# Performance work log

Measured on AMD Instinct MI355X. Metric: run time of the kernel, lower is better.

Reference implementation:

```python
import jax, jax.numpy as jnp
import numpy as np

N_NODES = 100000
N_EDGES = 3200000
N_FEAT = 128
DIM = 64
N_GRAPHS = 4096
EPS = 1e-5


def setup_inputs() -> dict:
    key = jax.random.key(0)
    ks = jax.random.split(key, 20)
    x = jax.random.normal(ks[0], (N_NODES, N_FEAT), dtype=jnp.float32)
    edge_index = jax.random.randint(ks[1], (2, N_EDGES), 0, N_NODES, dtype=jnp.int64)
    batch = jnp.sort(jax.random.randint(ks[2], (N_NODES,), 0, N_GRAPHS, dtype=jnp.int64))
    s = 0.1
    inp = {
        "x": x, "edge_index": edge_index, "batch": batch,
        "w1": jax.random.normal(ks[3], (N_FEAT, DIM), jnp.float32) * s,
        "b1": jnp.zeros((DIM,), jnp.float32),
        "bn1_g": 1.0 + s * jax.random.normal(ks[4], (DIM,), jnp.float32),
        "bn1_b": s * jax.random.normal(ks[5], (DIM,), jnp.float32),
        "conv_w": jax.random.normal(ks[6], (3, DIM, DIM), jnp.float32) * s,
        "conv_b": jnp.zeros((3, DIM), jnp.float32),
        "bnc_g": 1.0 + s * jax.random.normal(ks[7], (3, DIM), jnp.float32),
        "bnc_b": s * jax.random.normal(ks[8], (3, DIM), jnp.float32),
        "mlp_w": jax.random.normal(ks[9], (3, DIM, DIM), jnp.float32) * s,
        "mlp_b": jnp.zeros((3, DIM), jnp.float32),
        "bnm_g": 1.0 + s * jax.random.normal(ks[10], (3, DIM), jnp.float32),
        "bnm_b": s * jax.random.normal(ks[11], (3, DIM), jnp.float32),
        "out_w": jax.random.normal(ks[12], (DIM, 1), jnp.float32) * s,
        "out_b": jnp.zeros((1,), jnp.float32),
    }
    return inp


def _batchnorm(h, g, b):
    # training-mode BN: batch stats over the node/graph axis, biased variance
    m = jnp.mean(h, axis=0)
    v = jnp.var(h, axis=0)
    return (h - m) * jax.lax.rsqrt(v + EPS) * g + b


def _forward(x, edge_index, batch, w1, b1, bn1_g, bn1_b, conv_w, conv_b,
             bnc_g, bnc_b, mlp_w, mlp_b, bnm_g, bnm_b, out_w, out_b):
    src, dst = edge_index[0], edge_index[1]
    n = x.shape[0]
    # degree with self-loops (GCNConv default: add_self_loops=True, sym norm)
    deg = jax.ops.segment_sum(jnp.ones((src.shape[0],), x.dtype), dst, num_segments=n) + 1.0
    dis = jax.lax.rsqrt(deg)                  # D^{-1/2}
    enorm = (dis[src] * dis[dst])[:, None]    # per-edge norm [E,1]
    self_norm = (dis * dis)[:, None]          # self-loop norm = 1/deg [N,1]

    def gcn(h, W, b):
        h = h @ W                                                  # lin first (PyG)
        agg = jax.ops.segment_sum(h[src] * enorm, dst, num_segments=n)
        return agg + h * self_norm + b

    h = _batchnorm(jax.nn.relu(gcn(x, w1, b1)), bn1_g, bn1_b)
    for i in range(3):
        h = _batchnorm(gcn(h, conv_w[i], conv_b[i]), bnc_g[i], bnc_b[i])
    p = jax.ops.segment_sum(h, batch, num_segments=N_GRAPHS)       # global_add_pool
    for i in range(3):
        p = _batchnorm(jax.nn.relu(p @ mlp_w[i] + mlp_b[i]), bnm_g[i], bnm_b[i])
        # dropout: eval mode -> identity
    return p @ out_w + out_b


def reference(x, edge_index, batch, w1, b1, bn1_g, bn1_b, conv_w, conv_b,
              bnc_g, bnc_b, mlp_w, mlp_b, bnm_g, bnm_b, out_w, out_b):
    return _forward(x, edge_index, batch, w1, b1, bn1_g, bn1_b, conv_w, conv_b,
                    bnc_g, bnc_b, mlp_w, mlp_b, bnm_g, bnm_b, out_w, out_b)
```

## Files before the change

### kernel.cpp

```cpp
#include <hip/hip_runtime.h>
#include <hip/hip_bf16.h>

#define N_FEAT 128
#define DIM 64


__global__ void hist_kernel(const int* __restrict__ dst, int E, int* __restrict__ cnt) {
    int e = blockIdx.x * blockDim.x + threadIdx.x;
    if (e < E) atomicAdd(&cnt[dst[e]], 1);
}

__global__ void dis_kernel(const int* __restrict__ cnt, float* __restrict__ dis, int N) {
    int i = blockIdx.x * blockDim.x + threadIdx.x;
    if (i < N) dis[i] = rsqrtf((float)cnt[i] + 1.0f);
}

__global__ void scanA_kernel(const int* __restrict__ cnt, int N,
                             int* __restrict__ tmp, int* __restrict__ blk) {
    __shared__ int ts[256];
    int t = threadIdx.x;
    int base = blockIdx.x * 1024 + t * 4;
    int v[4];
    int s = 0;
#pragma unroll
    for (int j = 0; j < 4; j++) {
        int i = base + j;
        v[j] = (i < N) ? ((cnt[i] + 7) & ~7) : 0;
        s += v[j];
    }
    ts[t] = s;
    __syncthreads();
    for (int off = 1; off < 256; off <<= 1) {
        int x = (t >= off) ? ts[t - off] : 0;
        __syncthreads();
        ts[t] += x;
        __syncthreads();
    }
    int run = ts[t] - s;
#pragma unroll
    for (int j = 0; j < 4; j++) {
        run += v[j];
        int i = base + j;
        if (i < N) tmp[i] = run;
    }
    if (t == 255) blk[blockIdx.x] = ts[255];
}

__global__ void scanB_kernel(int* __restrict__ blk, int nb) {
    __shared__ int ts[128];
    int t = threadIdx.x;
    int v = (t < nb) ? blk[t] : 0;
    ts[t] = v;
    __syncthreads();
    for (int off = 1; off < 128; off <<= 1) {
        int x = (t >= off) ? ts[t - off] : 0;
        __syncthreads();
        ts[t] += x;
        __syncthreads();
    }
    if (t < nb) blk[t] = ts[t] - v;
}

__global__ void scanC_kernel(const int* __restrict__ tmp, const int* __restrict__ blk,
                             const int* __restrict__ cnt,
                             int N, int* __restrict__ rowp, int* __restrict__ cur) {
    int i = blockIdx.x * blockDim.x + threadIdx.x;
    if (i < N) {
        int b = i >> 10;
        int local = i & 1023;
        int excl = blk[b] + (local ? tmp[i - 1] : 0);
        rowp[i] = excl;
        cur[i] = excl;
        if (i == N - 1) rowp[N] = excl + ((cnt[i] + 7) & ~7);
    }
}

__global__ void fill_kernel(const int* __restrict__ src, const int* __restrict__ dst, int E,
                            const float* __restrict__ dis, int* __restrict__ cur,
                            int2* __restrict__ ecw) {
    int e = blockIdx.x * blockDim.x + threadIdx.x;
    if (e < E) {
        int s = src[e], d = dst[e];
        int pos = atomicAdd(&cur[d], 1);
        ecw[pos] = make_int2(s << 8, __float_as_int(dis[s] * dis[d]));
    }
}

__global__ void pad_kernel(const int* __restrict__ cur, const int* __restrict__ rowp,
                           int2* __restrict__ ecw, int N) {
    int i = blockIdx.x * blockDim.x + threadIdx.x;
    if (i < N) {
        int p = cur[i], e = rowp[i + 1];
        for (; p < e; p++) ecw[p] = make_int2(0, 0);
    }
}


template<int K, bool AFFINE, bool BIAS, bool RELU, bool STATS>
__global__ __launch_bounds__(256) void gemm_kernel(
    const float* __restrict__ A, const float* __restrict__ W,
    const float* __restrict__ scale, const float* __restrict__ shift,
    const float* __restrict__ bias, float* __restrict__ C,
    float* __restrict__ stats, int M)
{
    __shared__ float As[64][K + 4];
    __shared__ float Ws[K][64];
    __shared__ float bs[64], bq[64];
    int t = threadIdx.x;
    int row0 = blockIdx.x * 64;

    for (int q = t; q < K * 16; q += 256) {
        int k = q >> 4, c4 = (q & 15) << 2;
        float4 w = *reinterpret_cast<const float4*>(&W[k * 64 + c4]);
        *reinterpret_cast<float4*>(&Ws[k][c4]) = w;
    }
    for (int q = t; q < 64 * (K / 4); q += 256) {
        int r = q / (K / 4);
        int k4 = (q % (K / 4)) * 4;
        int row = row0 + r;
        float4 a;
        if (row < M) {
            a = *reinterpret_cast<const float4*>(&A[(size_t)row * K + k4]);
            if (AFFINE) {
                a.x = a.x * scale[k4]     + shift[k4];
                a.y = a.y * scale[k4 + 1] + shift[k4 + 1];
                a.z = a.z * scale[k4 + 2] + shift[k4 + 2];
                a.w = a.w * scale[k4 + 3] + shift[k4 + 3];
            }
        } else {
            a = make_float4(0.f, 0.f, 0.f, 0.f);
        }
        *reinterpret_cast<float4*>(&As[r][k4]) = a;
    }
    __syncthreads();

    int ty = t >> 4, tx = t & 15;
    int r0 = ty * 4, c0 = tx * 4;
    float acc[4][4] = {};
#pragma unroll 2
    for (int k = 0; k < K; k += 4) {
        float4 A0 = *reinterpret_cast<const float4*>(&As[r0 + 0][k]);
        float4 A1 = *reinterpret_cast<const float4*>(&As[r0 + 1][k]);
        float4 A2 = *reinterpret_cast<const float4*>(&As[r0 + 2][k]);
        float4 A3 = *reinterpret_cast<const float4*>(&As[r0 + 3][k]);
        float ar[4][4] = {{A0.x, A0.y, A0.z, A0.w}, {A1.x, A1.y, A1.z, A1.w},
                          {A2.x, A2.y, A2.z, A2.w}, {A3.x, A3.y, A3.z, A3.w}};
#pragma unroll
        for (int kk = 0; kk < 4; kk++) {
            float4 w = *reinterpret_cast<const float4*>(&Ws[k + kk][c0]);
#pragma unroll
            for (int i = 0; i < 4; i++) {
                acc[i][0] += ar[i][kk] * w.x;
                acc[i][1] += ar[i][kk] * w.y;
                acc[i][2] += ar[i][kk] * w.z;
                acc[i][3] += ar[i][kk] * w.w;
            }
        }
    }

    if (STATS) {
        if (t < 64) { bs[t] = 0.f; bq[t] = 0.f; }
        __syncthreads();
    }
    float ssum[4] = {0.f, 0.f, 0.f, 0.f}, ssq[4] = {0.f, 0.f, 0.f, 0.f};
#pragma unroll
    for (int i = 0; i < 4; i++) {
        int row = row0 + r0 + i;
        if (row < M) {
            float4 v;
            float* vp = &v.x;
#pragma unroll
            for (int j = 0; j < 4; j++) {
                float x = acc[i][j];
                if (BIAS) x += bias[c0 + j];
                if (RELU) x = fmaxf(x, 0.f);
                vp[j] = x;
                if (STATS) { ssum[j] += x; ssq[j] += x * x; }
            }
            *reinterpret_cast<float4*>(&C[(size_t)row * 64 + c0]) = v;
        }
    }
    if (STATS) {
#pragma unroll
        for (int j = 0; j < 4; j++) {
            atomicAdd(&bs[c0 + j], ssum[j]);
            atomicAdd(&bq[c0 + j], ssq[j]);
        }
        __syncthreads();
        if (t < 64) {
            atomicAdd(&stats[t], bs[t]);
            atomicAdd(&stats[64 + t], bq[t]);
        }
    }
}


template<bool RELU>
__global__ __launch_bounds__(256) void agg_kernel(
    const float* __restrict__ H, const int* __restrict__ rowp,
    const int2* __restrict__ ecw,
    const float* __restrict__ dis, const float* __restrict__ bias,
    float* __restrict__ Hout, float* __restrict__ stats, int N)
{
    __shared__ float bs[64], bq[64];
    int t = threadIdx.x;
    int lane = t & 63;
    unsigned lane4 = (unsigned)lane << 2;
    const char* Hb = (const char*)H;
    int base = (blockIdx.x * 4 + (t >> 6)) * 8;
    float b = bias[lane];
    float ssum = 0.f, ssq = 0.f;
    for (int u = 0; u < 8; u++) {
        int n = base + u;
        if (n >= N) break;
        int e0 = rowp[n], e1 = rowp[n + 1];
        float acc = 0.f;
        for (int e = e0; e < e1; e += 8) {
            int2 p[8];
#pragma unroll
            for (int j = 0; j < 8; j++) p[j] = ecw[e + j];
            float h[8];
#pragma unroll
            for (int j = 0; j < 8; j++)
                h[j] = *(const float*)(Hb + ((unsigned)p[j].x + lane4));
#pragma unroll
            for (int j = 0; j < 8; j++)
                acc += h[j] * __int_as_float(p[j].y);
        }
        float dn = dis[n];
        acc += H[(size_t)n * 64 + lane] * (dn * dn);
        acc += b;
        if (RELU) acc = fmaxf(acc, 0.f);
        Hout[(size_t)n * 64 + lane] = acc;
        ssum += acc;
        ssq += acc * acc;
    }
    if (t < 64) { bs[t] = 0.f; bq[t] = 0.f; }
    __syncthreads();
    atomicAdd(&bs[lane], ssum);
    atomicAdd(&bq[lane], ssq);
    __syncthreads();
    if (t < 64) {
        atomicAdd(&stats[t], bs[t]);
        atomicAdd(&stats[64 + t], bq[t]);
    }
}


__global__ void bnprep_kernel(const float* __restrict__ stats, const float* __restrict__ g,
                              const float* __restrict__ b, float* __restrict__ ss, float cntInv) {
    int c = threadIdx.x;
    float mean = stats[c] * cntInv;
    float var = stats[64 + c] * cntInv - mean * mean;
    float sc = g[c] * rsqrtf(var + 1e-5f);
    ss[c] = sc;
    ss[64 + c] = b[c] - mean * sc;
}


__global__ __launch_bounds__(256) void pool_kernel(
    const float* __restrict__ H, const int* __restrict__ batch,
    const float* __restrict__ ss, float* __restrict__ P, int N)
{
    int t = threadIdx.x;
    int lane = t & 63;
    int base = (blockIdx.x * 4 + (t >> 6)) * 8;
    float sc = ss[lane], sh = ss[64 + lane];
    float acc = 0.f;
    int gprev = -1;
    for (int u = 0; u < 8; u++) {
        int n = base + u;
        if (n >= N) break;
        int g = batch[n];
        if (g != gprev) {
            if (gprev >= 0) atomicAdd(&P[(size_t)gprev * 64 + lane], acc);
            acc = 0.f;
            gprev = g;
        }
        acc += H[(size_t)n * 64 + lane] * sc + sh;
    }
    if (gprev >= 0) atomicAdd(&P[(size_t)gprev * 64 + lane], acc);
}


__global__ __launch_bounds__(256) void final_kernel(
    const float* __restrict__ P, const float* __restrict__ ss,
    const float* __restrict__ outw, const float* __restrict__ outb,
    float* __restrict__ out, int G)
{
    int t = threadIdx.x;
    int lane = t & 63;
    int g = blockIdx.x * 4 + (t >> 6);
    if (g >= G) return;
    float v = (P[(size_t)g * 64 + lane] * ss[lane] + ss[64 + lane]) * outw[lane];
#pragma unroll
    for (int off = 32; off >= 1; off >>= 1) v += __shfl_xor(v, off, 64);
    if (lane == 0) out[g] = v + outb[0];
}


extern "C" void kernel_launch(void* const* d_in, const int* in_sizes, int n_in,
                              void* d_out, int out_size, void* d_ws, size_t ws_size,
                              hipStream_t stream)
{
    const float* x      = (const float*)d_in[0];
    const int*   ei     = (const int*)d_in[1];
    const int*   batch  = (const int*)d_in[2];
    const float* w1     = (const float*)d_in[3];
    const float* b1     = (const float*)d_in[4];
    const float* bn1_g  = (const float*)d_in[5];
    const float* bn1_b  = (const float*)d_in[6];
    const float* conv_w = (const float*)d_in[7];
    const float* conv_b = (const float*)d_in[8];
    const float* bnc_g  = (const float*)d_in[9];
    const float* bnc_b  = (const float*)d_in[10];
    const float* mlp_w  = (const float*)d_in[11];
    const float* mlp_b  = (const float*)d_in[12];
    const float* bnm_g  = (const float*)d_in[13];
    const float* bnm_b  = (const float*)d_in[14];
    const float* out_w  = (const float*)d_in[15];
    const float* out_b  = (const float*)d_in[16];
    float* out = (float*)d_out;

    const int N = in_sizes[0] / N_FEAT;
    const int E = in_sizes[1] / 2;
    const int G = out_size;
    const int* esrc = ei;
    const int* edst = ei + E;

    char* ws = (char*)d_ws;
    size_t off = 0;
    auto alloc = [&](size_t bytes) {
        size_t cur = off;
        off += (bytes + 255) & ~(size_t)255;
        return (void*)(ws + cur);
    };

    int*   deg   = (int*)alloc((size_t)N * 4);
    float* dis   = (float*)alloc((size_t)N * 4);
    int*   rtmp  = (int*)alloc((size_t)N * 4);
    int*   rowp  = (int*)alloc((size_t)(N + 1) * 4);
    int*   cur   = (int*)alloc((size_t)N * 4);
    int*   blk   = (int*)alloc(256 * 4);
    int2*  ecw   = (int2*)alloc(((size_t)E + 8ull * N) * 8);
    float* bufA  = (float*)alloc((size_t)(N + 64) * 64 * 4);
    float* bufB  = (float*)alloc((size_t)(N + 64) * 64 * 4);
    float* stats = (float*)alloc(7 * 128 * 4);
    float* ssbuf = (float*)alloc(7 * 128 * 4);
    float* P     = (float*)alloc((size_t)G * 64 * 4);
    float* pA    = (float*)alloc((size_t)G * 64 * 4);
    float* pB    = (float*)alloc((size_t)G * 64 * 4);

    hipMemsetAsync(deg, 0, (size_t)N * 4, stream);
    hipMemsetAsync(stats, 0, 7 * 128 * 4, stream);
    hipMemsetAsync(P, 0, (size_t)G * 64 * 4, stream);

    hist_kernel<<<(E + 255) / 256, 256, 0, stream>>>(edst, E, deg);
    dis_kernel<<<(N + 255) / 256, 256, 0, stream>>>(deg, dis, N);
    int nchunk = (N + 1023) / 1024;
    scanA_kernel<<<nchunk, 256, 0, stream>>>(deg, N, rtmp, blk);
    scanB_kernel<<<1, 128, 0, stream>>>(blk, nchunk);
    scanC_kernel<<<(N + 255) / 256, 256, 0, stream>>>(rtmp, blk, deg, N, rowp, cur);
    fill_kernel<<<(E + 255) / 256, 256, 0, stream>>>(esrc, edst, E, dis, cur, ecw);
    pad_kernel<<<(N + 255) / 256, 256, 0, stream>>>(cur, rowp, ecw, N);

    int gemmN_grid = (N + 63) / 64;
    int aggN_grid = (N + 31) / 32;

    gemm_kernel<128, false, false, false, false><<<gemmN_grid, 256, 0, stream>>>(
        x, w1, nullptr, nullptr, nullptr, bufA, nullptr, N);
    agg_kernel<true><<<aggN_grid, 256, 0, stream>>>(
        bufA, rowp, ecw, dis, b1, bufB, stats, N);
    bnprep_kernel<<<1, 64, 0, stream>>>(stats, bn1_g, bn1_b, ssbuf, 1.0f / N);

    for (int i = 0; i < 3; i++) {
        const float* W  = conv_w + (size_t)i * 64 * 64;
        const float* bb = conv_b + (size_t)i * 64;
        float* st     = stats + (size_t)(1 + i) * 128;
        float* ss_in  = ssbuf + (size_t)i * 128;
        float* ss_out = ssbuf + (size_t)(1 + i) * 128;
        gemm_kernel<64, true, false, false, false><<<gemmN_grid, 256, 0, stream>>>(
            bufB, W, ss_in, ss_in + 64, nullptr, bufA, nullptr, N);
        agg_kernel<false><<<aggN_grid, 256, 0, stream>>>(
            bufA, rowp, ecw, dis, bb, bufB, st, N);
        bnprep_kernel<<<1, 64, 0, stream>>>(st, bnc_g + (size_t)i * 64, bnc_b + (size_t)i * 64,
                                            ss_out, 1.0f / N);
    }

    pool_kernel<<<aggN_grid, 256, 0, stream>>>(bufB, batch, ssbuf + 3 * 128, P, N);

    int gemmG_grid = (G + 63) / 64;
    gemm_kernel<64, false, true, true, true><<<gemmG_grid, 256, 0, stream>>>(
        P, mlp_w, nullptr, nullptr, mlp_b, pA, stats + 4 * 128, G);
    bnprep_kernel<<<1, 64, 0, stream>>>(stats + 4 * 128, bnm_g, bnm_b, ssbuf + 4 * 128, 1.0f / G);

    gemm_kernel<64, true, true, true, true><<<gemmG_grid, 256, 0, stream>>>(
        pA, mlp_w + 64 * 64, ssbuf + 4 * 128, ssbuf + 4 * 128 + 64,
        mlp_b + 64, pB, stats + 5 * 128, G);
    bnprep_kernel<<<1, 64, 0, stream>>>(stats + 5 * 128, bnm_g + 64, bnm_b + 64, ssbuf + 5 * 128, 1.0f / G);

    gemm_kernel<64, true, true, true, true><<<gemmG_grid, 256, 0, stream>>>(
        pB, mlp_w + 2 * 64 * 64, ssbuf + 5 * 128, ssbuf + 5 * 128 + 64,
        mlp_b + 2 * 64, pA, stats + 6 * 128, G);
    bnprep_kernel<<<1, 64, 0, stream>>>(stats + 6 * 128, bnm_g + 2 * 64, bnm_b + 2 * 64, ssbuf + 6 * 128, 1.0f / G);

    final_kernel<<<(G + 3) / 4, 256, 0, stream>>>(pA, ssbuf + 6 * 128, out_w, out_b, out, G);
}
```

Baseline: 1.171 ms.

## Partition CSR fill by XCD and software-pipeline edge loads in aggregation

```diff
diff --git a/kernel.cpp b/kernel.cpp
--- a/kernel.cpp
+++ b/kernel.cpp
@@ -75,14 +75,24 @@
     }
 }
 
-__global__ void fill_kernel(const int* __restrict__ src, const int* __restrict__ dst, int E,
-                            const float* __restrict__ dis, int* __restrict__ cur,
-                            int2* __restrict__ ecw) {
-    int e = blockIdx.x * blockDim.x + threadIdx.x;
-    if (e < E) {
-        int s = src[e], d = dst[e];
-        int pos = atomicAdd(&cur[d], 1);
-        ecw[pos] = make_int2(s << 8, __float_as_int(dis[s] * dis[d]));
+#define NSLICE 256
+__global__ __launch_bounds__(256) void fill8_kernel(
+    const int* __restrict__ src, const int* __restrict__ dst, int E,
+    const float* __restrict__ dis, int* __restrict__ cur,
+    int2* __restrict__ ecw, int npx ) {
+    int xcd = blockIdx.x & 7;
+    int slice = blockIdx.x >> 3;
+    int per = (E + NSLICE - 1) / NSLICE;
+    int lo = slice * per;
+    int hi = min(lo + per, E);
+    int dlo = xcd * npx, dhi = dlo + npx;
+    for (int e = lo + threadIdx.x; e < hi; e += 256) {
+        int d = dst[e];
+        if (d >= dlo && d < dhi) {
+            int s = src[e];
+            int pos = atomicAdd(&cur[d], 1);
+            ecw[pos] = make_int2(s << 8, __float_as_int(dis[s] * dis[d]));
+        }
     }
 }
 
@@ -195,6 +205,21 @@
 }
 
 
+#define LOADP(P, ebase)                                     \
+    _Pragma("unroll") for (int j = 0; j < 4; j++)           \
+        P[j] = ecw4[((ebase) >> 1) + j];
+
+#define FMAG(P) {                                                          \
+    float h[8];                                                            \
+    _Pragma("unroll") for (int j = 0; j < 4; j++) {                        \
+        h[2*j]   = *(const float*)(Hb + ((unsigned)P[j].x + lane4));       \
+        h[2*j+1] = *(const float*)(Hb + ((unsigned)P[j].z + lane4));       \
+    }                                                                      \
+    _Pragma("unroll") for (int j = 0; j < 4; j++) {                        \
+        acc += h[2*j]   * __int_as_float(P[j].y);                          \
+        acc += h[2*j+1] * __int_as_float(P[j].w);                          \
+    } }
+
 template<bool RELU>
 __global__ __launch_bounds__(256) void agg_kernel(
     const float* __restrict__ H, const int* __restrict__ rowp,
@@ -203,6 +228,7 @@
     float* __restrict__ Hout, float* __restrict__ stats, int N)
 {
     __shared__ float bs[64], bq[64];
+    const int4* ecw4 = (const int4*)ecw;
     int t = threadIdx.x;
     int lane = t & 63;
     unsigned lane4 = (unsigned)lane << 2;
@@ -215,17 +241,19 @@
         if (n >= N) break;
         int e0 = rowp[n], e1 = rowp[n + 1];
         float acc = 0.f;
-        for (int e = e0; e < e1; e += 8) {
-            int2 p[8];
-#pragma unroll
-            for (int j = 0; j < 8; j++) p[j] = ecw[e + j];
-            float h[8];
-#pragma unroll
-            for (int j = 0; j < 8; j++)
-                h[j] = *(const float*)(Hb + ((unsigned)p[j].x + lane4));
-#pragma unroll
-            for (int j = 0; j < 8; j++)
-                acc += h[j] * __int_as_float(p[j].y);
+        int ng = (e1 - e0) >> 3;
+        if (ng > 0) {
+            int4 pa[4], pb[4];
+            int e = e0;
+            LOADP(pa, e);
+            int rem = ng - 1;
+            while (rem >= 2) {
+                LOADP(pb, e + 8); FMAG(pa);
+                LOADP(pa, e + 16); FMAG(pb);
+                e += 16; rem -= 2;
+            }
+            if (rem == 1) { LOADP(pb, e + 8); FMAG(pa); FMAG(pb); }
+            else { FMAG(pa); }
         }
         float dn = dis[n];
         acc += H[(size_t)n * 64 + lane] * (dn * dn);
@@ -361,7 +389,8 @@
     scanA_kernel<<<nchunk, 256, 0, stream>>>(deg, N, rtmp, blk);
     scanB_kernel<<<1, 128, 0, stream>>>(blk, nchunk);
     scanC_kernel<<<(N + 255) / 256, 256, 0, stream>>>(rtmp, blk, deg, N, rowp, cur);
-    fill_kernel<<<(E + 255) / 256, 256, 0, stream>>>(esrc, edst, E, dis, cur, ecw);
+    int npx = (N + 7) / 8;
+    fill8_kernel<<<NSLICE * 8, 256, 0, stream>>>(esrc, edst, E, dis, cur, ecw, npx);
     pad_kernel<<<(N + 255) / 256, 256, 0, stream>>>(cur, rowp, ecw, N);
 
     int gemmN_grid = (N + 63) / 64;
```

After: 1.131 ms. -3.4%, faster.
